# Kernel tuning notes

Hardware: AMD Instinct MI355X
Metric: run time of the kernel (lower is better)

## Reference

```python
import jax, jax.numpy as jnp
import numpy as np

MID = 256

def setup_inputs() -> dict:
    key = jax.random.key(0)
    ks = jax.random.split(key, 6)
    s = 1.0 / np.sqrt(MID)
    u = lambda k, shape: jax.random.uniform(k, shape, jnp.float32, -s, s)
    return {
        "W_ih": u(ks[0], (4 * MID, 2)),
        "W_hh": u(ks[1], (4 * MID, MID)),
        "b_ih": u(ks[2], (4 * MID,)),
        "b_hh": u(ks[3], (4 * MID,)),
        "W_out": u(ks[4], (1, MID)),
        "b_out": u(ks[5], (1,)),
        "sequence_dim": 48,
        "sequence_num": 512,
    }

def reference(W_ih, W_hh, b_ih, b_hh, W_out, b_out, sequence_dim, sequence_num):
    # obs is 2-D -> torch nn.LSTM treats it as UNBATCHED: (L=sequence_num, H_in=2),
    # hidden state (mid,) per layer, carried across outer iterations.
    N = sequence_num
    mid = W_hh.shape[1]
    b = b_ih + b_hh  # fuse the two LSTM biases

    def lstm(hc, obs):
        # obs: (N, 2) time-major unbatched sequence
        def step(carry, x):
            h, c = carry
            g = W_ih @ x + W_hh @ h + b          # (4*mid,)
            i, f, gg, o = jnp.split(g, 4)         # torch gate order i,f,g,o
            c = jax.nn.sigmoid(f) * c + jax.nn.sigmoid(i) * jnp.tanh(gg)
            h = jax.nn.sigmoid(o) * jnp.tanh(c)
            return (h, c), h
        hc, hs = jax.lax.scan(step, hc, obs)
        return hc, hs                              # hs: (N, mid)

    def outer(carry, k):
        hc, samp, prob = carry
        obs = jnp.concatenate([samp, prob], axis=1)  # (N, 2)
        hc, hs = lstm(hc, obs)
        p = jax.nn.sigmoid(hs @ W_out.T + b_out)     # (N, 1)
        smp = jax.random.bernoulli(k, p).astype(p.dtype)
        lp = smp * jnp.log(p) + (1.0 - smp) * jnp.log1p(-p)        # Bernoulli log_prob
        ent = -(p * jnp.log(p) + (1.0 - p) * jnp.log1p(-p))        # Bernoulli entropy
        return (hc, smp, p), (smp[:, 0], lp[:, 0], ent[:, 0])

    key = jax.random.key(42)
    keys = jax.random.split(key, sequence_dim - 1)
    h0 = (jnp.zeros((mid,), W_hh.dtype), jnp.zeros((mid,), W_hh.dtype))
    z = jnp.zeros((N, 1), W_hh.dtype)
    _, (ss, lps, ents) = jax.lax.scan(outer, (h0, z, z), keys)

    samples = jnp.concatenate([jnp.zeros((1, N), ss.dtype), ss], axis=0)  # (T, N)
    samples = samples.T.astype(jnp.int32)                                  # (N, T)
    logprobs = lps.sum(0)
    logprobs = logprobs - logprobs.mean()
    entropies = ents.mean(0)
    return samples, logprobs, entropies
```

## Files before the change

### kernel.cpp

```cpp
#include <hip/hip_runtime.h>
#include <stdint.h>


#define MID      256
#define NOUT     48
#define NSEQ     512
#define NOUTER   47
#define NSTEP    (NOUTER * NSEQ)
#define NBLK     16
#define MAGIC_V  0x1234ABCDu
#define LOG2E    1.4426950408889634f

#define LD_REL(p) __hip_atomic_load((p), __ATOMIC_RELAXED, __HIP_MEMORY_SCOPE_AGENT)

__device__ __forceinline__ uint32_t rotl32(uint32_t x, int d) {
  return (x << d) | (x >> (32 - d));
}

__device__ __forceinline__ void threefry2x32(uint32_t k0, uint32_t k1,
                                             uint32_t x0, uint32_t x1,
                                             uint32_t& o0, uint32_t& o1) {
  uint32_t ks2 = k0 ^ k1 ^ 0x1BD11BDAu;
  uint32_t v0 = x0 + k0, v1 = x1 + k1;
#define TF_R(r) { v0 += v1; v1 = rotl32(v1, r); v1 ^= v0; }
  TF_R(13) TF_R(15) TF_R(26) TF_R(6)
  v0 += k1;  v1 += ks2 + 1u;
  TF_R(17) TF_R(29) TF_R(16) TF_R(24)
  v0 += ks2; v1 += k0 + 2u;
  TF_R(13) TF_R(15) TF_R(26) TF_R(6)
  v0 += k0;  v1 += k1 + 3u;
  TF_R(17) TF_R(29) TF_R(16) TF_R(24)
  v0 += k1;  v1 += ks2 + 4u;
  TF_R(13) TF_R(15) TF_R(26) TF_R(6)
  v0 += ks2; v1 += k0 + 5u;
#undef TF_R
  o0 = v0; o1 = v1;
}

__device__ __forceinline__ float sigf(float x) { return 1.0f / (1.0f + expf(-x)); }

__device__ __forceinline__ uint64_t packht(float h, uint32_t tag) {
  return ((uint64_t)tag << 32) | (uint64_t)__float_as_uint(h);
}

__global__ __launch_bounds__(256, 1)
void arlstm_kernel(const float* __restrict__ W_ih, const float* __restrict__ W_hh,
                   const float* __restrict__ b_ih, const float* __restrict__ b_hh,
                   const float* __restrict__ W_out, const float* __restrict__ b_out,
                   float* __restrict__ out, uint64_t* __restrict__ ws) {
  uint64_t* h_hist = ws;
  float*    obsbuf = (float*)(ws + 512 * 256);
  uint32_t* p_prog = (uint32_t*)(obsbuf + 2 * 512 * 2);
  uint32_t* magic  = p_prog + 16;
  uint64_t* ob64   = (uint64_t*)obsbuf;

  const int tid = threadIdx.x;
  const int blk = blockIdx.x;

  __shared__ __align__(16) float hstage[2][256];
  __shared__ __align__(16) float ring[2][16][2];
  __shared__ float lp_acc[512];
  __shared__ float ent_acc[512];
  __shared__ float red[256];

  if (blk == NBLK) {
    __hip_atomic_store(&h_hist[tid], 0ull, __ATOMIC_RELAXED, __HIP_MEMORY_SCOPE_AGENT);
    if (tid < 16)
      __hip_atomic_store(&p_prog[tid], 0u, __ATOMIC_RELAXED, __HIP_MEMORY_SCOPE_AGENT);
    out[(tid)       * NOUT] = 0.0f;
    out[(tid + 256) * NOUT] = 0.0f;
    lp_acc[tid] = 0.0f;  lp_acc[tid + 256] = 0.0f;
    ent_acc[tid] = 0.0f; ent_acc[tid + 256] = 0.0f;
    __threadfence();
    __syncthreads();
    if (tid == 0)
      __hip_atomic_store(magic, MAGIC_V, __ATOMIC_RELEASE, __HIP_MEMORY_SCOPE_AGENT);

    const int w    = tid >> 6;
    const int lane = tid & 63;
    const float wo0 = W_out[lane * 4 + 0], wo1 = W_out[lane * 4 + 1];
    const float wo2 = W_out[lane * 4 + 2], wo3 = W_out[lane * 4 + 3];
    const float bo = b_out[0];

    for (int s = w + 1; s <= NSTEP; s += 4) {
      const int k = (s - 1) >> 9;
      const int t = (s - 1) & 511;
      uint64_t* src = h_hist + (uint64_t)(s & 511) * 256 + lane * 4;
      uint64_t v0, v1, v2, v3;
      for (;;) {
        v0 = LD_REL(src + 0);
        v1 = LD_REL(src + 1);
        v2 = LD_REL(src + 2);
        v3 = LD_REL(src + 3);
        int ok = ((uint32_t)(v0 >> 32) == (uint32_t)s) &
                 ((uint32_t)(v1 >> 32) == (uint32_t)s) &
                 ((uint32_t)(v2 >> 32) == (uint32_t)s) &
                 ((uint32_t)(v3 >> 32) == (uint32_t)s);
        if (__all(ok)) break;
      }
      float zp = fmaf(__uint_as_float((uint32_t)v0), wo0,
                 fmaf(__uint_as_float((uint32_t)v1), wo1,
                 fmaf(__uint_as_float((uint32_t)v2), wo2,
                      __uint_as_float((uint32_t)v3) * wo3)));
      zp += __shfl_xor(zp, 1);
      zp += __shfl_xor(zp, 2);
      zp += __shfl_xor(zp, 4);
      zp += __shfl_xor(zp, 8);
      zp += __shfl_xor(zp, 16);
      zp += __shfl_xor(zp, 32);
      const float p = sigf(zp + bo);

      uint32_t ka, kb, c1, c2;
      threefry2x32(0u, 42u, 0u, (uint32_t)k, ka, kb);
      threefry2x32(ka, kb, 0u, (uint32_t)t, c1, c2);
      const uint32_t bits = c1 ^ c2;
      const float u = __uint_as_float((bits >> 9) | 0x3f800000u) - 1.0f;
      const float smp = (u < p) ? 1.0f : 0.0f;

      if (lane == 0) {
        uint32_t* ob = (uint32_t*)(obsbuf + ((k + 1) & 1) * (512 * 2) + t * 2);
        __hip_atomic_store(&ob[0], __float_as_uint(smp), __ATOMIC_RELAXED, __HIP_MEMORY_SCOPE_AGENT);
        __hip_atomic_store(&ob[1], __float_as_uint(p),   __ATOMIC_RELAXED, __HIP_MEMORY_SCOPE_AGENT);
        __hip_atomic_store(&p_prog[w], (uint32_t)s, __ATOMIC_RELEASE, __HIP_MEMORY_SCOPE_AGENT);
        out[t * NOUT + (k + 1)] = smp;
        const float lg = logf(p), lg1 = log1pf(-p);
        lp_acc[t]  += (smp > 0.5f) ? lg : lg1;
        ent_acc[t] -= (p * lg + (1.0f - p) * lg1);
      }
    }
    __syncthreads();
    red[tid] = lp_acc[tid] + lp_acc[tid + 256];
    __syncthreads();
    for (int off = 128; off > 0; off >>= 1) {
      if (tid < off) red[tid] += red[tid + off];
      __syncthreads();
    }
    const float mean = red[0] * (1.0f / 512.0f);
    out[24576 + tid]        = lp_acc[tid]        - mean;
    out[24576 + 256 + tid]  = lp_acc[tid + 256]  - mean;
    out[25088 + tid]        = ent_acc[tid]       * (1.0f / 47.0f);
    out[25088 + 256 + tid]  = ent_acc[tid + 256] * (1.0f / 47.0f);
  } else {
    const int lane6 = tid & 63;
    const int wv    = tid >> 6;
    const int p     = lane6 & 3;
    const int js    = (lane6 >> 2) & 3;
    const int gate  = lane6 >> 4;
    const int jl    = 4 * wv + js;
    const int jglob = blk * 16 + jl;
    const int rr    = gate * 256 + blk * 16 + jl;

    float wreg[64];
#pragma unroll
    for (int c = 0; c < 64; ++c)
      wreg[c] = W_hh[rr * 256 + p * 64 + c];

    const float bb  = b_ih[rr] + b_hh[rr];
    const float wx0 = W_ih[rr * 2 + 0];
    const float wx1 = W_ih[rr * 2 + 1];
    const float mconst = (gate == 2) ? (-2.0f * LOG2E) : (-LOG2E);
    const float ml     = (gate == 2) ? 2.0f : 1.0f;
    const float ad     = (gate == 2) ? -1.0f : 0.0f;

    if (tid < 16) {
      ring[0][tid][0] = 0.f; ring[0][tid][1] = 0.f;
      ring[1][tid][0] = 0.f; ring[1][tid][1] = 0.f;
    }

    if (tid == 0) {
      while (__hip_atomic_load(magic, __ATOMIC_ACQUIRE, __HIP_MEMORY_SCOPE_AGENT) != MAGIC_V) {}
    }
    __syncthreads();

    float c_st = 0.0f;
    const bool own = (tid >= blk * 16) && (tid < blk * 16 + 16);

    int      pf_tgt = 0, pf_need = 0;
    uint32_t pf_ppv = 0;
    uint64_t pf_ov  = 0;

    for (int s = 1; s <= NSTEP; ++s) {
      const int ph = (s - 1) & 15;

      if (wv == 3) {
        if (ph == 0) {
          pf_tgt  = s + 16 + lane6;
          pf_need = 0;
          if (lane6 < 16 && pf_tgt > NSEQ && pf_tgt <= NSTEP) {
            pf_need = pf_tgt - NSEQ;
            pf_ppv  = LD_REL(&p_prog[(pf_need - 1) & 3]);
          }
        } else if (ph == 1) {
          bool ok = (pf_need == 0) || (pf_ppv >= (uint32_t)pf_need);
          while (!__all(ok)) {
            if (!ok) pf_ppv = LD_REL(&p_prog[(pf_need - 1) & 3]);
            ok = (pf_need == 0) || (pf_ppv >= (uint32_t)pf_need);
          }
          pf_ov = 0;
          if (lane6 < 16 && pf_need != 0) {
            const int kk = (pf_tgt - 1) >> 9;
            const int tt = (pf_tgt - 1) & 511;
            pf_ov = LD_REL(ob64 + (kk & 1) * 512 + tt);
          }
        } else if (ph == 2) {
          if (lane6 < 16) {
            const int par = (((s - 3) >> 4) + 1) & 1;
            ring[par][lane6][0] = __uint_as_float((uint32_t)pf_ov);
            ring[par][lane6][1] = __uint_as_float((uint32_t)(pf_ov >> 32));
          }
        }
      }

      if (s == 1 || !own) {
        uint64_t* src = h_hist + (uint64_t)((s - 1) & 511) * 256 + tid;
        const uint32_t want = (uint32_t)(s - 1);
        uint64_t v = LD_REL(src);
        if ((uint32_t)(v >> 32) != want) {
          uint64_t q0 = LD_REL(src), q1 = LD_REL(src);
          uint64_t q2 = LD_REL(src), q3 = LD_REL(src);
          for (;;) {
            if ((uint32_t)(q0 >> 32) == want) { v = q0; break; }
            q0 = LD_REL(src);
            if ((uint32_t)(q1 >> 32) == want) { v = q1; break; }
            q1 = LD_REL(src);
            if ((uint32_t)(q2 >> 32) == want) { v = q2; break; }
            q2 = LD_REL(src);
            if ((uint32_t)(q3 >> 32) == want) { v = q3; break; }
            q3 = LD_REL(src);
          }
        }
        hstage[s & 1][tid] = __uint_as_float((uint32_t)v);
      }
      __syncthreads();

      float a0 = 0.f, a1 = 0.f, a2 = 0.f, a3 = 0.f;
      const float4* hs4 = (const float4*)&hstage[s & 1][p * 64];
#pragma unroll
      for (int i = 0; i < 16; ++i) {
        const float4 hv = hs4[i];
        a0 = fmaf(wreg[4 * i + 0], hv.x, a0);
        a1 = fmaf(wreg[4 * i + 1], hv.y, a1);
        a2 = fmaf(wreg[4 * i + 2], hv.z, a2);
        a3 = fmaf(wreg[4 * i + 3], hv.w, a3);
      }
      float gp = (a0 + a1) + (a2 + a3);
      gp += __shfl_xor(gp, 1);
      gp += __shfl_xor(gp, 2);

      const float sx = ring[((s - 1) >> 4) & 1][ph][0];
      const float px = ring[((s - 1) >> 4) & 1][ph][1];
      const float gv = gp + (wx0 * sx + wx1 * px + bb);

      const float e   = __builtin_amdgcn_exp2f(gv * mconst);
      const float y   = __builtin_amdgcn_rcpf(1.0f + e);
      const float act = __builtin_fmaf(ml, y, ad);

      const float a_f = __shfl(act, (lane6 & 15) + 16, 64);
      const float a_g = __shfl(act, (lane6 & 15) + 32, 64);
      const float a_o = __shfl(act, (lane6 & 15) + 48, 64);

      if (lane6 < 16) {
        const float t1 = a_f * c_st;
        const float t2 = act * a_g;
        c_st = t1 + t2;
        const float ec = __builtin_amdgcn_exp2f(c_st * (-2.0f * LOG2E));
        const float yc = __builtin_amdgcn_rcpf(1.0f + ec);
        const float th = __builtin_fmaf(2.0f, yc, -1.0f);
        const float hnew = a_o * th;
        if (p == 0) {
          hstage[(s + 1) & 1][jglob] = hnew;
          __hip_atomic_store(&h_hist[(uint64_t)(s & 511) * 256 + jglob],
                             packht(hnew, (uint32_t)s),
                             __ATOMIC_RELAXED, __HIP_MEMORY_SCOPE_AGENT);
        }
      }
    }
  }
}

extern "C" void kernel_launch(void* const* d_in, const int* in_sizes, int n_in,
                              void* d_out, int out_size, void* d_ws, size_t ws_size,
                              hipStream_t stream) {
  const float* W_ih  = (const float*)d_in[0];
  const float* W_hh  = (const float*)d_in[1];
  const float* b_ih  = (const float*)d_in[2];
  const float* b_hh  = (const float*)d_in[3];
  const float* W_out = (const float*)d_in[4];
  const float* b_out = (const float*)d_in[5];
  float* out = (float*)d_out;
  uint64_t* ws = (uint64_t*)d_ws;

  arlstm_kernel<<<dim3(NBLK + 1), dim3(256), 0, stream>>>(
      W_ih, W_hh, b_ih, b_hh, W_out, b_out, out, ws);
}
```

Measured before the change: 39.33 ms.

## Split matvec K-dimension across waves with LDS reduction, single hstage buffer

Each wave now handles one quarter of the K dimension for all 64 gate rows of the block, and partial sums are reduced through an LDS array. The previous layout instead had each wave own 4 hidden units and reduce with lane shuffles. Only wave 0 computes the activations and the cell update, which removes the redundant activation work done on the other three waves. The change also drops the double-buffered hstage and uses a custom waitcnt+s_barrier macro. The cost is a second block barrier per step and more LDS traffic on the serial critical path.

```diff
diff --git a/kernel.cpp b/kernel.cpp
--- a/kernel.cpp
+++ b/kernel.cpp
@@ -11,7 +11,14 @@
 #define MAGIC_V  0x1234ABCDu
 #define LOG2E    1.4426950408889634f
 
+typedef __attribute__((ext_vector_type(4))) float f32x4;
+
 #define LD_REL(p) __hip_atomic_load((p), __ATOMIC_RELAXED, __HIP_MEMORY_SCOPE_AGENT)
+
+#define LDS_BARRIER() do {                                          \
+    asm volatile("s_waitcnt lgkmcnt(0)\n\ts_barrier" ::: "memory"); \
+    __builtin_amdgcn_sched_barrier(0);                              \
+  } while (0)
 
 __device__ __forceinline__ uint32_t rotl32(uint32_t x, int d) {
   return (x << d) | (x >> (32 - d));
@@ -57,8 +64,9 @@
   const int tid = threadIdx.x;
   const int blk = blockIdx.x;
 
-  __shared__ __align__(16) float hstage[2][256];
-  __shared__ __align__(16) float ring[2][16][2];
+  __shared__ __align__(16) float hstage[256];
+  __shared__ float plds[4][64];
+  __shared__ float ring[2][16][2];
   __shared__ float lp_acc[512];
   __shared__ float ent_acc[512];
   __shared__ float red[256];
@@ -141,26 +149,30 @@
     out[25088 + tid]        = ent_acc[tid]       * (1.0f / 47.0f);
     out[25088 + 256 + tid]  = ent_acc[tid + 256] * (1.0f / 47.0f);
   } else {
-    const int lane6 = tid & 63;
-    const int wv    = tid >> 6;
-    const int p     = lane6 & 3;
-    const int js    = (lane6 >> 2) & 3;
-    const int gate  = lane6 >> 4;
-    const int jl    = 4 * wv + js;
-    const int jglob = blk * 16 + jl;
-    const int rr    = gate * 256 + blk * 16 + jl;
-
-    float wreg[64];
+    const int part = tid >> 6;
+    const int r    = tid & 63;
+    const int gate = r >> 4;
+    const int jloc = r & 15;
+    const int row  = gate * 256 + blk * 16 + jloc;
+
+    f32x4 w4[16];
+    const f32x4* wsrc = (const f32x4*)(W_hh + row * 256 + part * 64);
 #pragma unroll
-    for (int c = 0; c < 64; ++c)
-      wreg[c] = W_hh[rr * 256 + p * 64 + c];
-
-    const float bb  = b_ih[rr] + b_hh[rr];
-    const float wx0 = W_ih[rr * 2 + 0];
-    const float wx1 = W_ih[rr * 2 + 1];
-    const float mconst = (gate == 2) ? (-2.0f * LOG2E) : (-LOG2E);
-    const float ml     = (gate == 2) ? 2.0f : 1.0f;
-    const float ad     = (gate == 2) ? -1.0f : 0.0f;
+    for (int i = 0; i < 16; ++i) w4[i] = wsrc[i];
+#pragma unroll
+    for (int i = 0; i < 16; ++i) asm volatile("" : "+v"(w4[i]));
+
+    float bb = 0.f, wx0 = 0.f, wx1 = 0.f, mconst = 0.f, ml = 0.f, ad = 0.f;
+    if (tid < 64) {
+      const int g4 = tid >> 4;
+      const int rr = g4 * 256 + blk * 16 + (tid & 15);
+      bb  = b_ih[rr] + b_hh[rr];
+      wx0 = W_ih[rr * 2 + 0];
+      wx1 = W_ih[rr * 2 + 1];
+      mconst = (g4 == 2) ? (-2.0f * LOG2E) : (-LOG2E);
+      ml     = (g4 == 2) ? 2.0f : 1.0f;
+      ad     = (g4 == 2) ? -1.0f : 0.0f;
+    }
 
     if (tid < 16) {
       ring[0][tid][0] = 0.f; ring[0][tid][1] = 0.f;
@@ -173,6 +185,7 @@
     __syncthreads();
 
     float c_st = 0.0f;
+    const int jglob = blk * 16 + (tid & 15);
     const bool own = (tid >= blk * 16) && (tid < blk * 16 + 16);
 
     int      pf_tgt = 0, pf_need = 0;
@@ -182,11 +195,11 @@
     for (int s = 1; s <= NSTEP; ++s) {
       const int ph = (s - 1) & 15;
 
-      if (wv == 3) {
+      if (part == 3) {
         if (ph == 0) {
-          pf_tgt  = s + 16 + lane6;
+          pf_tgt  = s + 16 + r;
           pf_need = 0;
-          if (lane6 < 16 && pf_tgt > NSEQ && pf_tgt <= NSTEP) {
+          if (r < 16 && pf_tgt > NSEQ && pf_tgt <= NSTEP) {
             pf_need = pf_tgt - NSEQ;
             pf_ppv  = LD_REL(&p_prog[(pf_need - 1) & 3]);
           }
@@ -197,16 +210,16 @@
             ok = (pf_need == 0) || (pf_ppv >= (uint32_t)pf_need);
           }
           pf_ov = 0;
-          if (lane6 < 16 && pf_need != 0) {
+          if (r < 16 && pf_need != 0) {
             const int kk = (pf_tgt - 1) >> 9;
             const int tt = (pf_tgt - 1) & 511;
             pf_ov = LD_REL(ob64 + (kk & 1) * 512 + tt);
           }
         } else if (ph == 2) {
-          if (lane6 < 16) {
+          if (r < 16) {
             const int par = (((s - 3) >> 4) + 1) & 1;
-            ring[par][lane6][0] = __uint_as_float((uint32_t)pf_ov);
-            ring[par][lane6][1] = __uint_as_float((uint32_t)(pf_ov >> 32));
+            ring[par][r][0] = __uint_as_float((uint32_t)pf_ov);
+            ring[par][r][1] = __uint_as_float((uint32_t)(pf_ov >> 32));
           }
         }
       }
@@ -229,46 +242,45 @@
             q3 = LD_REL(src);
           }
         }
-        hstage[s & 1][tid] = __uint_as_float((uint32_t)v);
-      }
-      __syncthreads();
+        hstage[tid] = __uint_as_float((uint32_t)v);
+      }
+      LDS_BARRIER();
 
       float a0 = 0.f, a1 = 0.f, a2 = 0.f, a3 = 0.f;
-      const float4* hs4 = (const float4*)&hstage[s & 1][p * 64];
+      const f32x4* hs4 = (const f32x4*)(hstage + part * 64);
 #pragma unroll
       for (int i = 0; i < 16; ++i) {
-        const float4 hv = hs4[i];
-        a0 = fmaf(wreg[4 * i + 0], hv.x, a0);
-        a1 = fmaf(wreg[4 * i + 1], hv.y, a1);
-        a2 = fmaf(wreg[4 * i + 2], hv.z, a2);
-        a3 = fmaf(wreg[4 * i + 3], hv.w, a3);
-      }
-      float gp = (a0 + a1) + (a2 + a3);
-      gp += __shfl_xor(gp, 1);
-      gp += __shfl_xor(gp, 2);
-
-      const float sx = ring[((s - 1) >> 4) & 1][ph][0];
-      const float px = ring[((s - 1) >> 4) & 1][ph][1];
-      const float gv = gp + (wx0 * sx + wx1 * px + bb);
-
-      const float e   = __builtin_amdgcn_exp2f(gv * mconst);
-      const float y   = __builtin_amdgcn_rcpf(1.0f + e);
-      const float act = __builtin_fmaf(ml, y, ad);
-
-      const float a_f = __shfl(act, (lane6 & 15) + 16, 64);
-      const float a_g = __shfl(act, (lane6 & 15) + 32, 64);
-      const float a_o = __shfl(act, (lane6 & 15) + 48, 64);
-
-      if (lane6 < 16) {
-        const float t1 = a_f * c_st;
-        const float t2 = act * a_g;
-        c_st = t1 + t2;
-        const float ec = __builtin_amdgcn_exp2f(c_st * (-2.0f * LOG2E));
-        const float yc = __builtin_amdgcn_rcpf(1.0f + ec);
-        const float th = __builtin_fmaf(2.0f, yc, -1.0f);
-        const float hnew = a_o * th;
-        if (p == 0) {
-          hstage[(s + 1) & 1][jglob] = hnew;
+        const f32x4 hv = hs4[i];
+        a0 = fmaf(w4[i][0], hv[0], a0);
+        a1 = fmaf(w4[i][1], hv[1], a1);
+        a2 = fmaf(w4[i][2], hv[2], a2);
+        a3 = fmaf(w4[i][3], hv[3], a3);
+      }
+      plds[part][r] = (a0 + a1) + (a2 + a3);
+      LDS_BARRIER();
+
+      if (tid < 64) {
+        const float sx = ring[((s - 1) >> 4) & 1][ph][0];
+        const float px = ring[((s - 1) >> 4) & 1][ph][1];
+        const float base = wx0 * sx + wx1 * px + bb;
+        const float gv = ((plds[0][tid] + plds[1][tid]) +
+                          (plds[2][tid] + plds[3][tid])) + base;
+        const float e   = __builtin_amdgcn_exp2f(gv * mconst);
+        const float y   = __builtin_amdgcn_rcpf(1.0f + e);
+        const float act = __builtin_fmaf(ml, y, ad);
+        const int j = tid & 15;
+        const float a_f = __shfl(act, j + 16, 64);
+        const float a_g = __shfl(act, j + 32, 64);
+        const float a_o = __shfl(act, j + 48, 64);
+        if (tid < 16) {
+          const float t1 = a_f * c_st;
+          const float t2 = act * a_g;
+          c_st = t1 + t2;
+          const float ec = __builtin_amdgcn_exp2f(c_st * (-2.0f * LOG2E));
+          const float yc = __builtin_amdgcn_rcpf(1.0f + ec);
+          const float th = __builtin_fmaf(2.0f, yc, -1.0f);
+          const float hnew = a_o * th;
+          hstage[jglob] = hnew;
           __hip_atomic_store(&h_hist[(uint64_t)(s & 511) * 256 + jglob],
                              packht(hnew, (uint32_t)s),
                              __ATOMIC_RELAXED, __HIP_MEMORY_SCOPE_AGENT);
```

After: 32.57 ms. 1.21x faster.
